# Optimization experiments

Hardware: AMD Instinct MI355X
Metric: run time of the kernel (lower is better)

The kernel has to match this reference:

```python
import jax, jax.numpy as jnp
import numpy as np

HEADS = 16
HEAD_DIM = 64
LN_EPS = 1e-5


def setup_inputs() -> dict:
    key = jax.random.key(0)
    k_x, k_q, k_k, k_v = jax.random.split(key, 4)
    B, C, H, W = 32, 640, 32, 32
    inner = HEADS * HEAD_DIM  # 1024
    x = jax.random.normal(k_x, (B, C, H, W), dtype=jnp.float32)
    # nn.Linear(in_dim, inner_dim, bias=False): weight shape [inner, in_dim]
    Wq = jax.random.normal(k_q, (inner, C), dtype=jnp.float32) * 0.02
    Wk = jax.random.normal(k_k, (inner, C), dtype=jnp.float32) * 0.02
    Wv = jax.random.normal(k_v, (inner, C), dtype=jnp.float32) * 0.02
    # out_norm = nn.LayerNorm(head_dim): default init gamma=1, beta=0
    gamma = jnp.ones((HEAD_DIM,), dtype=jnp.float32)
    beta = jnp.zeros((HEAD_DIM,), dtype=jnp.float32)
    return {"x": x, "Wq": Wq, "Wk": Wk, "Wv": Wv, "gamma": gamma, "beta": beta}


def _layernorm(y, gamma, beta):
    mu = jnp.mean(y, axis=-1, keepdims=True)
    var = jnp.mean(jnp.square(y - mu), axis=-1, keepdims=True)
    return (y - mu) * jax.lax.rsqrt(var + LN_EPS) * gamma + beta


def reference(x, Wq, Wk, Wv, gamma, beta):
    B, C, H, W = x.shape
    N = H * W
    scale = HEAD_DIM ** -0.5
    # rearrange 'b c h w -> b (h w) c' (patch_size=1)
    t = x.reshape(B, C, N).transpose(0, 2, 1)  # [B, N, C]
    def proj(Wm):
        p = jnp.einsum('bnc,ec->bne', t, Wm)  # [B, N, inner]
        return p.reshape(B, N, HEADS, HEAD_DIM).transpose(0, 2, 1, 3)  # [B, h, N, d]
    q, k, v = proj(Wq), proj(Wk), proj(Wv)
    qk = jnp.einsum('bhid,bhjd->bhij', q, k)  # [B, h, N, N]
    p_att = jax.nn.softmax(qk * scale, axis=-1)
    out = jnp.einsum('bhij,bhjd->bhid', p_att, v)  # [B, h, N, d]
    out = out.mean(axis=2)  # [B, h, d]
    return _layernorm(out, gamma, beta)
```

## Files before the change

kernel.cpp:

```cpp
#include <hip/hip_runtime.h>
#include <hip/hip_bf16.h>

typedef __bf16 bf16;
typedef __bf16 bf16x8 __attribute__((ext_vector_type(8)));
typedef float f32x4 __attribute__((ext_vector_type(4)));

#define QSCALE 0.18033688011112042f

#define EXP2(x) __builtin_amdgcn_exp2f(x)

__device__ __forceinline__ void load_lds16(const void* gp, void* lp) {
  __builtin_amdgcn_global_load_lds((const __attribute__((address_space(1))) void*)gp,
                                   (__attribute__((address_space(3))) void*)lp, 16, 0, 0);
}

__global__ __launch_bounds__(256) void k_transpose(const float* __restrict__ x,
                                                   bf16* __restrict__ t) {
  __shared__ float tile[64][65];
  const int b = blockIdx.z, c0 = blockIdx.y * 64, n0 = blockIdx.x * 64;
  const int tid = threadIdx.x, lx = tid & 63, ly = tid >> 6;
  const float* xp = x + ((size_t)b * 640 + c0) * 1024 + n0;
#pragma unroll
  for (int i = 0; i < 16; ++i) {
    int c = i * 4 + ly;
    tile[c][lx] = xp[(size_t)c * 1024 + lx];
  }
  __syncthreads();
  bf16* tp = t + ((size_t)b * 1024 + n0) * 640 + c0;
#pragma unroll
  for (int i = 0; i < 16; ++i) {
    int n = i * 4 + ly;
    tp[(size_t)n * 640 + lx] = (bf16)tile[lx][n];
  }
}

__global__ __launch_bounds__(256) void k_castw3(const float* __restrict__ wq,
                                                const float* __restrict__ wk,
                                                const float* __restrict__ wv,
                                                bf16* __restrict__ dst) {
  int i = blockIdx.x * 256 + threadIdx.x;
  if (i < 655360) dst[i] = (bf16)(wq[i] * QSCALE);
  else if (i < 1310720) dst[i] = (bf16)wk[i - 655360];
  else if (i < 1966080) dst[i] = (bf16)wv[i - 1310720];
}

__global__ __launch_bounds__(256) void k_gemm_qkv(const bf16* __restrict__ A,
                                                  const bf16* __restrict__ Bw,
                                                  bf16* __restrict__ qkv) {
  __shared__ __align__(16) bf16 smem[2][2][8192];
  const int tid = threadIdx.x;
  const int lane = tid & 63;
  const int w = tid >> 6;
  const int wm = w & 1, wn = w >> 1;
  const int g = lane >> 4, ln = lane & 15;
  const int m0 = blockIdx.x * 128;
  const int n0 = blockIdx.y * 128;

  f32x4 acc[4][4];
#pragma unroll
  for (int i = 0; i < 4; ++i)
#pragma unroll
    for (int j = 0; j < 4; ++j)
#pragma unroll
      for (int r = 0; r < 4; ++r) acc[i][j][r] = 0.f;

#define GSTAGE(buf, kt)                                                        \
  do {                                                                         \
    _Pragma("unroll") for (int it_ = 0; it_ < 4; ++it_) {                      \
      int c_ = it_ * 256 + w * 64 + lane;                                      \
      int m_ = c_ >> 3;                                                        \
      int kq_ = (c_ & 7) ^ (m_ & 7);                                           \
      load_lds16(A + (size_t)(m0 + m_) * 640 + ((kt) * 64 + kq_ * 8),          \
                 &smem[buf][0][(size_t)(it_ * 256 + w * 64) * 8]);             \
      load_lds16(Bw + (size_t)(n0 + m_) * 640 + ((kt) * 64 + kq_ * 8),        \
                 &smem[buf][1][(size_t)(it_ * 256 + w * 64) * 8]);             \
    }                                                                          \
  } while (0)

  GSTAGE(0, 0);
  for (int kt = 0; kt < 10; ++kt) {
    const int cur = kt & 1;
    __syncthreads();
    if (kt + 1 < 10) GSTAGE(1 - cur, kt + 1);
    const bf16* As = smem[cur][0];
    const bf16* Bs = smem[cur][1];
#pragma unroll
    for (int kk = 0; kk < 2; ++kk) {
      bf16x8 af[4], bfr[4];
#pragma unroll
      for (int mi = 0; mi < 4; ++mi) {
        int m = wm * 64 + mi * 16 + ln;
        int cc = m * 8 + ((kk * 4 + g) ^ (m & 7));
        af[mi] = *(const bf16x8*)(As + cc * 8);
      }
#pragma unroll
      for (int ni = 0; ni < 4; ++ni) {
        int n = wn * 64 + ni * 16 + ln;
        int cc = n * 8 + ((kk * 4 + g) ^ (n & 7));
        bfr[ni] = *(const bf16x8*)(Bs + cc * 8);
      }
#pragma unroll
      for (int mi = 0; mi < 4; ++mi)
#pragma unroll
        for (int ni = 0; ni < 4; ++ni)
          acc[mi][ni] = __builtin_amdgcn_mfma_f32_16x16x32_bf16(af[mi], bfr[ni], acc[mi][ni], 0, 0, 0);
    }
  }
#undef GSTAGE

  __syncthreads();
  bf16* ct = &smem[0][0][0];
#pragma unroll
  for (int mi = 0; mi < 4; ++mi)
#pragma unroll
    for (int ni = 0; ni < 4; ++ni)
#pragma unroll
      for (int r = 0; r < 4; ++r) {
        int row = wm * 64 + mi * 16 + g * 4 + r;
        int col = wn * 64 + ni * 16 + ln;
        ct[row * 136 + col] = (bf16)acc[mi][ni][r];
      }
  __syncthreads();
  const int which = n0 >> 10;
  const int hbase = (n0 >> 6) & 15;
#pragma unroll
  for (int p = 0; p < 8; ++p) {
    int row = p * 16 + (tid >> 4);
    int chunk = tid & 15;
    bf16x8 vv = *(const bf16x8*)(ct + row * 136 + chunk * 8);
    int gr = m0 + row;
    int bb = gr >> 10, n = gr & 1023;
    int h = hbase + (chunk >> 3);
    int d0 = (chunk & 7) * 8;
    *(bf16x8*)(qkv + (size_t)which * 33554432 +
               (((size_t)bb * 16 + h) * 1024 + n) * 64 + d0) = vv;
  }
}

__global__ __launch_bounds__(256) void k_attn(const bf16* __restrict__ q,
                                              const bf16* __restrict__ kmat,
                                              float* __restrict__ wsum) {
  __shared__ __align__(16) bf16 Ks[2][4096];
  const int idx = blockIdx.x;
  const int xcd = idx & 7;
  const int y = idx >> 3;
  const int it = y & 3;
  const int bh = xcd + ((y >> 2) << 3);
  const int tid = threadIdx.x;
  const int lane = tid & 63;
  const int w = tid >> 6;
  const int g = lane >> 4, ln = lane & 15;
  const bf16* qb = q + (size_t)bh * 65536;
  const bf16* kb = kmat + (size_t)bh * 65536;
  const int i0 = it * 256 + w * 64;

  const f32x4 zf = {0.f, 0.f, 0.f, 0.f};

#define STAGEK(buf, jt)                                                       \
  do {                                                                        \
    _Pragma("unroll") for (int call_ = 0; call_ < 2; ++call_) {               \
      int p_ = w * 128 + call_ * 64 + lane;                                   \
      int j_ = p_ >> 3;                                                       \
      int kq_ = (p_ & 7) ^ (j_ & 7);                                          \
      load_lds16(kb + (size_t)((jt) * 64 + j_) * 64 + kq_ * 8,                \
                 &Ks[buf][(size_t)(w * 128 + call_ * 64) * 8]);               \
    }                                                                         \
  } while (0)

#define KFRAG(buf, ni, kc)                                                    \
  (*(const bf16x8*)(&Ks[buf][(size_t)(((ni) * 16 + ln) * 8 +                  \
                                      (((kc) * 4 + g) ^ (ln & 7))) * 8]))

  bf16x8 qf[4][2];
#pragma unroll
  for (int mi = 0; mi < 4; ++mi)
#pragma unroll
    for (int kc = 0; kc < 2; ++kc)
      qf[mi][kc] = *(const bf16x8*)(qb + (size_t)(i0 + mi * 16 + ln) * 64 + kc * 32 + g * 8);

  float rs[4][4];
#pragma unroll
  for (int mi = 0; mi < 4; ++mi)
#pragma unroll
    for (int r = 0; r < 4; ++r) rs[mi][r] = 0.f;

  STAGEK(0, 0);
  for (int jt = 0; jt < 16; ++jt) {
    const int cur = jt & 1;
    __syncthreads();
    if (jt + 1 < 16) STAGEK(1 - cur, jt + 1);
    bf16x8 kf[4][2];
#pragma unroll
    for (int ni = 0; ni < 4; ++ni)
#pragma unroll
      for (int kc = 0; kc < 2; ++kc) kf[ni][kc] = KFRAG(cur, ni, kc);
#pragma unroll
    for (int mi = 0; mi < 4; ++mi)
#pragma unroll
      for (int ni = 0; ni < 4; ++ni) {
        f32x4 s = __builtin_amdgcn_mfma_f32_16x16x32_bf16(qf[mi][0], kf[ni][0], zf, 0, 0, 0);
        s = __builtin_amdgcn_mfma_f32_16x16x32_bf16(qf[mi][1], kf[ni][1], s, 0, 0, 0);
#pragma unroll
        for (int r = 0; r < 4; ++r) rs[mi][r] += EXP2(s[r]);
      }
  }
  float rinv[4][4];
#pragma unroll
  for (int mi = 0; mi < 4; ++mi)
#pragma unroll
    for (int r = 0; r < 4; ++r) {
      float v = rs[mi][r];
      v += __shfl_xor(v, 1);
      v += __shfl_xor(v, 2);
      v += __shfl_xor(v, 4);
      v += __shfl_xor(v, 8);
      rinv[mi][r] = 1.0f / v;
    }

  STAGEK(0, 0);
  for (int jt = 0; jt < 16; ++jt) {
    const int cur = jt & 1;
    __syncthreads();
    if (jt + 1 < 16) STAGEK(1 - cur, jt + 1);
    bf16x8 kf[4][2];
#pragma unroll
    for (int ni = 0; ni < 4; ++ni)
#pragma unroll
      for (int kc = 0; kc < 2; ++kc) kf[ni][kc] = KFRAG(cur, ni, kc);
    float cs[4] = {0.f, 0.f, 0.f, 0.f};
#pragma unroll
    for (int mi = 0; mi < 4; ++mi)
#pragma unroll
      for (int ni = 0; ni < 4; ++ni) {
        f32x4 s = __builtin_amdgcn_mfma_f32_16x16x32_bf16(qf[mi][0], kf[ni][0], zf, 0, 0, 0);
        s = __builtin_amdgcn_mfma_f32_16x16x32_bf16(qf[mi][1], kf[ni][1], s, 0, 0, 0);
#pragma unroll
        for (int r = 0; r < 4; ++r) cs[ni] += EXP2(s[r]) * rinv[mi][r];
      }
#pragma unroll
    for (int ni = 0; ni < 4; ++ni) {
      float v = cs[ni];
      v += __shfl_xor(v, 16);
      v += __shfl_xor(v, 32);
      if (g == 0) atomicAdd(wsum + (size_t)bh * 1024 + jt * 64 + ni * 16 + ln, v);
    }
  }
#undef STAGEK
#undef KFRAG
}

__global__ __launch_bounds__(256) void k_final(const float* __restrict__ wsum,
                                               const bf16* __restrict__ v,
                                               const float* __restrict__ gamma,
                                               const float* __restrict__ beta,
                                               float* __restrict__ out) {
  const int bh = blockIdx.x;
  const int tid = threadIdx.x;
  const int d = tid & 63, part = tid >> 6;
  const bf16* vb = v + (size_t)bh * 65536;
  const float* wb = wsum + (size_t)bh * 1024;
  float acc = 0.f;
  for (int j = part * 256; j < part * 256 + 256; ++j)
    acc += wb[j] * (float)vb[(size_t)j * 64 + d];
  __shared__ float red[4][64];
  red[part][d] = acc;
  __syncthreads();
  if (tid < 64) {
    float y = (red[0][d] + red[1][d] + red[2][d] + red[3][d]) * (1.0f / 1024.0f);
    float s1 = y;
#pragma unroll
    for (int off = 1; off < 64; off <<= 1) s1 += __shfl_xor(s1, off);
    float mu = s1 * (1.0f / 64.0f);
    float dy = y - mu;
    float s2 = dy * dy;
#pragma unroll
    for (int off = 1; off < 64; off <<= 1) s2 += __shfl_xor(s2, off);
    float rstd = rsqrtf(s2 * (1.0f / 64.0f) + 1e-5f);
    out[(size_t)bh * 64 + d] = dy * rstd * gamma[d] + beta[d];
  }
}

extern "C" void kernel_launch(void* const* d_in, const int* in_sizes, int n_in,
                              void* d_out, int out_size, void* d_ws, size_t ws_size,
                              hipStream_t stream) {
  const float* x     = (const float*)d_in[0];
  const float* Wq    = (const float*)d_in[1];
  const float* Wk    = (const float*)d_in[2];
  const float* Wv    = (const float*)d_in[3];
  const float* gamma = (const float*)d_in[4];
  const float* beta  = (const float*)d_in[5];
  float* out = (float*)d_out;

  char* ws = (char*)d_ws;
  bf16*  tbf  = (bf16*)ws;
  bf16*  wbf  = (bf16*)(ws + 41943040);
  bf16*  qkv  = (bf16*)(ws + 45875200);
  float* wsum = (float*)(ws + 247201792);

  hipMemsetAsync(wsum, 0, (size_t)512 * 1024 * sizeof(float), stream);
  k_transpose<<<dim3(16, 10, 32), 256, 0, stream>>>(x, tbf);
  k_castw3<<<7680, 256, 0, stream>>>(Wq, Wk, Wv, wbf);
  k_gemm_qkv<<<dim3(256, 24), 256, 0, stream>>>(tbf, wbf, qkv);
  k_attn<<<2048, 256, 0, stream>>>(qkv, qkv + 33554432, wsum);
  k_final<<<512, 256, 0, stream>>>(wsum, qkv + 67108864, gamma, beta, out);
}
```

Baseline: 481.6 us.

## Cache exp scores in FP8 registers to skip second QK pass

The attention kernel previously ran two full QK^T passes, the first for row sums and the second to recompute exponentials for column-weighted sums. It now computes each score once, packs the exponentials into FP8 registers (16x2x4 words per thread) and reuses them after the row normalisers are known. This removes the second K staging and MFMA pass. To fit the register cache, each wave handles 32 query rows instead of 64, the grid doubles to 4096 blocks, and launch bounds request 2 blocks per SM. FP8 quantisation of the exponentials adds error to the softmax weights, and the per-column atomics to wsum are doubled.

New measurement: 1.018 ms. +111.3%, slower.

```diff
diff --git a/kernel.cpp b/kernel.cpp
--- a/kernel.cpp
+++ b/kernel.cpp
@@ -137,22 +137,22 @@
   }
 }
 
-__global__ __launch_bounds__(256) void k_attn(const bf16* __restrict__ q,
-                                              const bf16* __restrict__ kmat,
-                                              float* __restrict__ wsum) {
+__global__ __launch_bounds__(256, 2) void k_attn(const bf16* __restrict__ q,
+                                                 const bf16* __restrict__ kmat,
+                                                 float* __restrict__ wsum) {
   __shared__ __align__(16) bf16 Ks[2][4096];
   const int idx = blockIdx.x;
   const int xcd = idx & 7;
   const int y = idx >> 3;
-  const int it = y & 3;
-  const int bh = xcd + ((y >> 2) << 3);
+  const int it = y & 7;
+  const int bh = xcd + ((y >> 3) << 3);
   const int tid = threadIdx.x;
   const int lane = tid & 63;
   const int w = tid >> 6;
   const int g = lane >> 4, ln = lane & 15;
   const bf16* qb = q + (size_t)bh * 65536;
   const bf16* kb = kmat + (size_t)bh * 65536;
-  const int i0 = it * 256 + w * 64;
+  const int i0 = it * 128 + w * 32;
 
   const f32x4 zf = {0.f, 0.f, 0.f, 0.f};
 
@@ -171,42 +171,46 @@
   (*(const bf16x8*)(&Ks[buf][(size_t)(((ni) * 16 + ln) * 8 +                  \
                                       (((kc) * 4 + g) ^ (ln & 7))) * 8]))
 
-  bf16x8 qf[4][2];
-#pragma unroll
-  for (int mi = 0; mi < 4; ++mi)
+  bf16x8 qf[2][2];
+#pragma unroll
+  for (int mi = 0; mi < 2; ++mi)
 #pragma unroll
     for (int kc = 0; kc < 2; ++kc)
       qf[mi][kc] = *(const bf16x8*)(qb + (size_t)(i0 + mi * 16 + ln) * 64 + kc * 32 + g * 8);
 
-  float rs[4][4];
-#pragma unroll
-  for (int mi = 0; mi < 4; ++mi)
+  float rs[2][4];
+#pragma unroll
+  for (int mi = 0; mi < 2; ++mi)
 #pragma unroll
     for (int r = 0; r < 4; ++r) rs[mi][r] = 0.f;
 
+  unsigned es[16][2][4];
+
   STAGEK(0, 0);
+#pragma unroll
   for (int jt = 0; jt < 16; ++jt) {
     const int cur = jt & 1;
     __syncthreads();
     if (jt + 1 < 16) STAGEK(1 - cur, jt + 1);
-    bf16x8 kf[4][2];
-#pragma unroll
-    for (int ni = 0; ni < 4; ++ni)
-#pragma unroll
-      for (int kc = 0; kc < 2; ++kc) kf[ni][kc] = KFRAG(cur, ni, kc);
-#pragma unroll
-    for (int mi = 0; mi < 4; ++mi)
-#pragma unroll
-      for (int ni = 0; ni < 4; ++ni) {
-        f32x4 s = __builtin_amdgcn_mfma_f32_16x16x32_bf16(qf[mi][0], kf[ni][0], zf, 0, 0, 0);
-        s = __builtin_amdgcn_mfma_f32_16x16x32_bf16(qf[mi][1], kf[ni][1], s, 0, 0, 0);
-#pragma unroll
-        for (int r = 0; r < 4; ++r) rs[mi][r] += EXP2(s[r]);
-      }
-  }
-  float rinv[4][4];
-#pragma unroll
-  for (int mi = 0; mi < 4; ++mi)
+#pragma unroll
+    for (int ni = 0; ni < 4; ++ni) {
+      bf16x8 k0 = KFRAG(cur, ni, 0);
+      bf16x8 k1 = KFRAG(cur, ni, 1);
+#pragma unroll
+      for (int mi = 0; mi < 2; ++mi) {
+        f32x4 s = __builtin_amdgcn_mfma_f32_16x16x32_bf16(qf[mi][0], k0, zf, 0, 0, 0);
+        s = __builtin_amdgcn_mfma_f32_16x16x32_bf16(qf[mi][1], k1, s, 0, 0, 0);
+        float e0 = EXP2(s[0]), e1 = EXP2(s[1]), e2 = EXP2(s[2]), e3 = EXP2(s[3]);
+        rs[mi][0] += e0; rs[mi][1] += e1; rs[mi][2] += e2; rs[mi][3] += e3;
+        int p = __builtin_amdgcn_cvt_pk_fp8_f32(e0, e1, 0, false);
+        p = __builtin_amdgcn_cvt_pk_fp8_f32(e2, e3, p, true);
+        es[jt][mi][ni] = (unsigned)p;
+      }
+    }
+  }
+  float rinv[2][4];
+#pragma unroll
+  for (int mi = 0; mi < 2; ++mi)
 #pragma unroll
     for (int r = 0; r < 4; ++r) {
       float v = rs[mi][r];
@@ -217,32 +221,22 @@
       rinv[mi][r] = 1.0f / v;
     }
 
-  STAGEK(0, 0);
+#pragma unroll
   for (int jt = 0; jt < 16; ++jt) {
-    const int cur = jt & 1;
-    __syncthreads();
-    if (jt + 1 < 16) STAGEK(1 - cur, jt + 1);
-    bf16x8 kf[4][2];
-#pragma unroll
-    for (int ni = 0; ni < 4; ++ni)
-#pragma unroll
-      for (int kc = 0; kc < 2; ++kc) kf[ni][kc] = KFRAG(cur, ni, kc);
-    float cs[4] = {0.f, 0.f, 0.f, 0.f};
-#pragma unroll
-    for (int mi = 0; mi < 4; ++mi)
-#pragma unroll
-      for (int ni = 0; ni < 4; ++ni) {
-        f32x4 s = __builtin_amdgcn_mfma_f32_16x16x32_bf16(qf[mi][0], kf[ni][0], zf, 0, 0, 0);
-        s = __builtin_amdgcn_mfma_f32_16x16x32_bf16(qf[mi][1], kf[ni][1], s, 0, 0, 0);
-#pragma unroll
-        for (int r = 0; r < 4; ++r) cs[ni] += EXP2(s[r]) * rinv[mi][r];
-      }
 #pragma unroll
     for (int ni = 0; ni < 4; ++ni) {
-      float v = cs[ni];
-      v += __shfl_xor(v, 16);
-      v += __shfl_xor(v, 32);
-      if (g == 0) atomicAdd(wsum + (size_t)bh * 1024 + jt * 64 + ni * 16 + ln, v);
+      float cs = 0.f;
+#pragma unroll
+      for (int mi = 0; mi < 2; ++mi) {
+        const unsigned E = es[jt][mi][ni];
+        cs += __builtin_amdgcn_cvt_f32_fp8(E, 0) * rinv[mi][0];
+        cs += __builtin_amdgcn_cvt_f32_fp8(E, 1) * rinv[mi][1];
+        cs += __builtin_amdgcn_cvt_f32_fp8(E, 2) * rinv[mi][2];
+        cs += __builtin_amdgcn_cvt_f32_fp8(E, 3) * rinv[mi][3];
+      }
+      cs += __shfl_xor(cs, 16);
+      cs += __shfl_xor(cs, 32);
+      if (g == 0) atomicAdd(wsum + (size_t)bh * 1024 + jt * 64 + ni * 16 + ln, cs);
     }
   }
 #undef STAGEK
@@ -297,10 +291,10 @@
   bf16*  qkv  = (bf16*)(ws + 45875200);
   float* wsum = (float*)(ws + 247201792);
 
-  hipMemsetAsync(wsum, 0, (size_t)512 * 1024 * sizeof(float), stream);
+  (void)hipMemsetAsync(wsum, 0, (size_t)512 * 1024 * sizeof(float), stream);
   k_transpose<<<dim3(16, 10, 32), 256, 0, stream>>>(x, tbf);
   k_castw3<<<7680, 256, 0, stream>>>(Wq, Wk, Wv, wbf);
   k_gemm_qkv<<<dim3(256, 24), 256, 0, stream>>>(tbf, wbf, qkv);
-  k_attn<<<2048, 256, 0, stream>>>(qkv, qkv + 33554432, wsum);
+  k_attn<<<4096, 256, 0, stream>>>(qkv, qkv + 33554432, wsum);
   k_final<<<512, 256, 0, stream>>>(wsum, qkv + 67108864, gamma, beta, out);
 }
```
